# Optimization experiments

Hardware: AMD Instinct MI355X
Metric: run time of the kernel (lower is better)

## Reference

```python
import jax, jax.numpy as jnp
import numpy as np

B, D_IN, D_H, D_OUT = 1024, 1024, 4096, 1024
SPARSITY = 0.5  # fraction of weights KEPT (top-k)


def setup_inputs() -> dict:
    key = jax.random.key(0)
    ks = jax.random.split(key, 13)
    def kaiming(k, shape):
        fan_in = shape[-1] if len(shape) > 1 else shape[0]
        bound = 1.0 / np.sqrt(fan_in)
        return jax.random.uniform(k, shape, jnp.float32, -bound, bound)
    inp = {
        "x":   jax.random.normal(ks[0], (B, D_IN), jnp.float32),
        "W1":  kaiming(ks[1], (D_H, D_IN)),
        "b1":  kaiming(ks[2], (D_H,)),
        "W2":  kaiming(ks[3], (D_H, D_H)),
        "b2":  kaiming(ks[4], (D_H,)),
        "W3":  kaiming(ks[5], (D_OUT, D_H)),
        "b3":  kaiming(ks[6], (D_OUT,)),
        # scores: kaiming-uniform for weights, N(0, 0.01) for biases (as in Mask.__init__)
        "sW1": kaiming(ks[7], (D_H, D_IN)),
        "sb1": 0.01 * jax.random.normal(ks[8], (D_H,), jnp.float32),
        "sW2": kaiming(ks[9], (D_H, D_H)),
        "sb2": 0.01 * jax.random.normal(ks[10], (D_H,), jnp.float32),
        "sW3": kaiming(ks[11], (D_OUT, D_H)),
        "sb3": 0.01 * jax.random.normal(ks[12], (D_OUT,), jnp.float32),
    }
    return inp


def _global_masks(scores):
    """Single fused global top-k threshold mask (replaces O(P) redundant sorts).
    Bottom (1-SPARSITY) fraction (by value rank) -> 0, top SPARSITY fraction -> 1."""
    flat = jnp.concatenate([s.ravel() for s in scores])
    n = flat.shape[0]
    j = int((1.0 - SPARSITY) * n)  # number of zeroed entries
    idx = jnp.argsort(flat)
    bin_mask = jnp.zeros((n,), flat.dtype).at[idx[j:]].set(1.0)
    # straight-through: d(mask)/d(score) = 1 (GetSubnet_global.backward returns g)
    st_mask = bin_mask + flat - jax.lax.stop_gradient(flat)
    sizes = [int(np.prod(s.shape)) for s in scores]
    offs = np.concatenate([[0], np.cumsum(sizes)])
    return [st_mask[offs[i]:offs[i + 1]].reshape(scores[i].shape)
            for i in range(len(scores))]


def reference(x, W1, b1, W2, b2, W3, b3, sW1, sb1, sW2, sb2, sW3, sb3):
    masks = _global_masks([sW1, sb1, sW2, sb2, sW3, sb3])
    mW1, mb1, mW2, mb2, mW3, mb3 = masks
    # masked params, then MLP forward (torch Linear: y = x @ W.T + b)
    h = jax.nn.relu(x @ (W1 * mW1).T + b1 * mb1)
    h = jax.nn.relu(h @ (W2 * mW2).T + b2 * mb2)
    return h @ (W3 * mW3).T + b3 * mb3
```

## Files before the change

### kernel.cpp

```cpp
#include <hip/hip_runtime.h>
#include <hip/hip_bf16.h>
#include <stdint.h>


typedef __bf16 bf16_t;
typedef __bf16 bf16x4 __attribute__((ext_vector_type(4)));
typedef __bf16 bf16x8 __attribute__((ext_vector_type(8)));
typedef float  f32x4  __attribute__((ext_vector_type(4)));

using gvoid = const __attribute__((address_space(1))) void;
using svoid = __attribute__((address_space(3))) void;

#define O1 4194304L
#define O2 4198400L
#define O3 20975616L
#define O4 20979712L
#define O5 25174016L
#define N_TOT 25175040L
#define J_RANK 12587520u
#define CAND_CAP 4096

#define HIST_BLOCKS 512

#define WS_HIST 0u
#define WS_RES  32768u
#define WS_CNT  32784u
#define WS_CAND 32800u
#define WS_W1B  131072u
#define WS_B1F  8519680u
#define WS_W2B  8536064u
#define WS_B2F  42090496u
#define WS_W3B  42106880u
#define WS_B3F  50495488u
#define WS_H1F  50511872u
#define WS_H2F  58900480u
#define WS_FAST_END 67289088ull
#define WS_H1   131072u
#define WS_H2   8519680u

#define SWZ(row, chunk) ((((chunk) + ((row) >> 1)) & 3))

__device__ __forceinline__ unsigned int mono32(float f) {
    unsigned int u = __float_as_uint(f);
    return (u & 0x80000000u) ? ~u : (u | 0x80000000u);
}

__global__ __launch_bounds__(256) void zero_kernel(unsigned int* p, int n) {
    int i = blockIdx.x * 256 + threadIdx.x;
    if (i < n) p[i] = 0u;
}

__global__ __launch_bounds__(256) void cvt_x_kernel(const float* __restrict__ x,
                                                    bf16_t* __restrict__ xb, int n8) {
    int i = blockIdx.x * 256 + threadIdx.x;
    if (i < n8) {
        const float4 a = *(const float4*)(x + (size_t)i * 8);
        const float4 b = *(const float4*)(x + (size_t)i * 8 + 4);
        bf16x8 r;
        r[0] = (__bf16)a.x; r[1] = (__bf16)a.y; r[2] = (__bf16)a.z; r[3] = (__bf16)a.w;
        r[4] = (__bf16)b.x; r[5] = (__bf16)b.y; r[6] = (__bf16)b.z; r[7] = (__bf16)b.w;
        *(bf16x8*)(xb + (size_t)i * 8) = r;
    }
}

__device__ __forceinline__ void seg_lookup(long e,
    const float* s0, const float* s1, const float* s2,
    const float* s3, const float* s4, const float* s5,
    const float** sp, long* off) {
    if (e < O1)      { *sp = s0; *off = e; }
    else if (e < O2) { *sp = s1; *off = e - O1; }
    else if (e < O3) { *sp = s2; *off = e - O2; }
    else if (e < O4) { *sp = s3; *off = e - O3; }
    else if (e < O5) { *sp = s4; *off = e - O4; }
    else             { *sp = s5; *off = e - O5; }
}

__global__ __launch_bounds__(256) void hist_kernel(
    const float* s0, const float* s1, const float* s2,
    const float* s3, const float* s4, const float* s5,
    unsigned int* hb) {
    __shared__ unsigned int lh[8192];
    for (int i = threadIdx.x; i < 8192; i += 256) lh[i] = 0u;
    __syncthreads();
    const long ng = N_TOT / 4;
    for (long g = (long)blockIdx.x * 256 + threadIdx.x; g < ng;
         g += (long)gridDim.x * 256) {
        long e = g * 4;
        const float* sp; long o;
        seg_lookup(e, s0, s1, s2, s3, s4, s5, &sp, &o);
        float4 v = *(const float4*)(sp + o);
        atomicAdd(&lh[mono32(v.x) >> 19], 1u);
        atomicAdd(&lh[mono32(v.y) >> 19], 1u);
        atomicAdd(&lh[mono32(v.z) >> 19], 1u);
        atomicAdd(&lh[mono32(v.w) >> 19], 1u);
    }
    __syncthreads();
    unsigned int* dst = hb + (size_t)blockIdx.x * 8192;
    for (int i = threadIdx.x; i < 8192; i += 256) dst[i] = lh[i];
}

__global__ __launch_bounds__(256) void reduce_hist(const unsigned int* __restrict__ hb,
                                                   unsigned int* __restrict__ hist) {
    int b = blockIdx.x * 256 + threadIdx.x;
    unsigned int s = 0;
    for (int blk = 0; blk < HIST_BLOCKS; ++blk)
        s += hb[(size_t)blk * 8192 + b];
    hist[b] = s;
}

__global__ __launch_bounds__(256) void select_kernel(const unsigned int* hist,
                                                     unsigned int* res) {
    __shared__ unsigned int part[256];
    int tid = threadIdx.x;
    unsigned int s = 0;
    for (int b = tid * 32; b < tid * 32 + 32; ++b) s += hist[b];
    part[tid] = s;
    __syncthreads();
    if (tid == 0) {
        unsigned int acc = 0;
        for (int i = 0; i < 256; ++i) { unsigned int v = part[i]; part[i] = acc; acc += v; }
    }
    __syncthreads();
    unsigned int acc = part[tid];
    for (int b = tid * 32; b < tid * 32 + 32; ++b) {
        unsigned int h = hist[b];
        if (acc <= J_RANK && J_RANK < acc + h) {
            res[0] = (unsigned int)b;
            res[1] = acc;
            res[2] = J_RANK - acc;
        }
        acc += h;
    }
}

__global__ __launch_bounds__(256) void mask_apply_fast(
    const float* s0, const float* s1, const float* s2,
    const float* s3, const float* s4, const float* s5,
    const float* w0, const float* w1, const float* w2,
    const float* w3, const float* w4, const float* w5,
    bf16_t* W1b, float* b1f, bf16_t* W2b, float* b2f, bf16_t* W3b, float* b3f,
    const unsigned int* res, unsigned int* cand_cnt, unsigned long long* cand) {
    const unsigned int C = res[0];
    const long ng = N_TOT / 4;
    for (long g = (long)blockIdx.x * 256 + threadIdx.x; g < ng;
         g += (long)gridDim.x * 256) {
        long e = g * 4;
        const float* sp; long o;
        seg_lookup(e, s0, s1, s2, s3, s4, s5, &sp, &o);
        const float* wp;
        if (e < O1)      wp = w0;
        else if (e < O2) wp = w1;
        else if (e < O3) wp = w2;
        else if (e < O4) wp = w3;
        else if (e < O5) wp = w4;
        else             wp = w5;
        float4 sv = *(const float4*)(sp + o);
        float4 wv = *(const float4*)(wp + o);
#define PROC(comp, ci)                                                         \
        { unsigned int key = mono32(sv.comp); unsigned int kb = key >> 19;     \
          if (kb < C) wv.comp = 0.f;                                           \
          else if (kb == C) {                                                  \
              unsigned int slot = atomicAdd(cand_cnt, 1u);                     \
              if (slot < CAND_CAP)                                             \
                  cand[slot] = (((unsigned long long)key) << 32) |             \
                               (unsigned long long)(unsigned int)(e + ci);     \
          } }
        PROC(x, 0) PROC(y, 1) PROC(z, 2) PROC(w, 3)
#undef PROC
        if (e < O1) {
            bf16x4 b; b[0]=(__bf16)wv.x; b[1]=(__bf16)wv.y; b[2]=(__bf16)wv.z; b[3]=(__bf16)wv.w;
            *(bf16x4*)(W1b + o) = b;
        } else if (e < O2) {
            *(float4*)(b1f + o) = wv;
        } else if (e < O3) {
            bf16x4 b; b[0]=(__bf16)wv.x; b[1]=(__bf16)wv.y; b[2]=(__bf16)wv.z; b[3]=(__bf16)wv.w;
            *(bf16x4*)(W2b + o) = b;
        } else if (e < O4) {
            *(float4*)(b2f + o) = wv;
        } else if (e < O5) {
            bf16x4 b; b[0]=(__bf16)wv.x; b[1]=(__bf16)wv.y; b[2]=(__bf16)wv.z; b[3]=(__bf16)wv.w;
            *(bf16x4*)(W3b + o) = b;
        } else {
            *(float4*)(b3f + o) = wv;
        }
    }
}

__global__ __launch_bounds__(256) void finalize_fast(
    const unsigned int* res, const unsigned int* cand_cnt,
    const unsigned long long* cand,
    bf16_t* W1b, float* b1f, bf16_t* W2b, float* b2f, bf16_t* W3b, float* b3f) {
    __shared__ unsigned long long buf[CAND_CAP];
    int tid = threadIdx.x;
    unsigned int cnt = *cand_cnt; if (cnt > CAND_CAP) cnt = CAND_CAP;
    unsigned int need = res[2];   if (need > cnt) need = cnt;
    for (int i = tid; i < (int)cnt; i += 256) buf[i] = cand[i];
    __syncthreads();
    for (int i = tid; i < (int)cnt; i += 256) {
        unsigned long long me = buf[i];
        unsigned int rank = 0;
        for (unsigned int j = 0; j < cnt; ++j) rank += (buf[j] < me);
        if (rank < need) {
            long idx = (long)(unsigned int)(me & 0xFFFFFFFFu);
            if (idx < O1)      W1b[idx] = (__bf16)0.f;
            else if (idx < O2) b1f[idx - O1] = 0.f;
            else if (idx < O3) W2b[idx - O2] = (__bf16)0.f;
            else if (idx < O4) b2f[idx - O3] = 0.f;
            else if (idx < O5) W3b[idx - O4] = (__bf16)0.f;
            else               b3f[idx - O5] = 0.f;
        }
    }
}

__global__ __launch_bounds__(256) void mask_apply_kernel(
    const float* s0, const float* s1, const float* s2,
    const float* s3, const float* s4, const float* s5,
    float* w0, float* w1, float* w2, float* w3, float* w4, float* w5,
    const unsigned int* res, unsigned int* cand_cnt, unsigned long long* cand) {
    const unsigned int C = res[0];
    const long ng = N_TOT / 4;
    for (long g = (long)blockIdx.x * 256 + threadIdx.x; g < ng;
         g += (long)gridDim.x * 256) {
        long e = g * 4;
        const float* sp; long o;
        seg_lookup(e, s0, s1, s2, s3, s4, s5, &sp, &o);
        float* wp;
        if (e < O1)      wp = w0;
        else if (e < O2) wp = w1;
        else if (e < O3) wp = w2;
        else if (e < O4) wp = w3;
        else if (e < O5) wp = w4;
        else             wp = w5;
        float4 sv = *(const float4*)(sp + o);
        float4 wv = *(float4*)(wp + o);
#define PROC(comp, ci)                                                         \
        { unsigned int key = mono32(sv.comp); unsigned int kb = key >> 19;     \
          if (kb < C) wv.comp = 0.f;                                           \
          else if (kb == C) {                                                  \
              unsigned int slot = atomicAdd(cand_cnt, 1u);                     \
              if (slot < CAND_CAP)                                             \
                  cand[slot] = (((unsigned long long)key) << 32) |             \
                               (unsigned long long)(unsigned int)(e + ci);     \
          } }
        PROC(x, 0) PROC(y, 1) PROC(z, 2) PROC(w, 3)
#undef PROC
        *(float4*)(wp + o) = wv;
    }
}

__global__ __launch_bounds__(256) void finalize_kernel(
    const unsigned int* res, const unsigned int* cand_cnt,
    const unsigned long long* cand,
    float* w0, float* w1, float* w2, float* w3, float* w4, float* w5) {
    __shared__ unsigned long long buf[CAND_CAP];
    int tid = threadIdx.x;
    unsigned int cnt = *cand_cnt; if (cnt > CAND_CAP) cnt = CAND_CAP;
    unsigned int need = res[2];   if (need > cnt) need = cnt;
    for (int i = tid; i < (int)cnt; i += 256) buf[i] = cand[i];
    __syncthreads();
    for (int i = tid; i < (int)cnt; i += 256) {
        unsigned long long me = buf[i];
        unsigned int rank = 0;
        for (unsigned int j = 0; j < cnt; ++j) rank += (buf[j] < me);
        if (rank < need) {
            long idx = (long)(unsigned int)(me & 0xFFFFFFFFu);
            if (idx < O1)      w0[idx] = 0.f;
            else if (idx < O2) w1[idx - O1] = 0.f;
            else if (idx < O3) w2[idx - O2] = 0.f;
            else if (idx < O4) w3[idx - O3] = 0.f;
            else if (idx < O5) w4[idx - O4] = 0.f;
            else               w5[idx - O5] = 0.f;
        }
    }
}

__device__ __forceinline__ bf16x8 load8(const float* p) {
    float4 a = *(const float4*)p;
    float4 b = *(const float4*)(p + 4);
    bf16x8 r;
    r[0] = (__bf16)a.x; r[1] = (__bf16)a.y; r[2] = (__bf16)a.z; r[3] = (__bf16)a.w;
    r[4] = (__bf16)b.x; r[5] = (__bf16)b.y; r[6] = (__bf16)b.z; r[7] = (__bf16)b.w;
    return r;
}
__device__ __forceinline__ bf16x8 load8(const bf16_t* p) {
    return *(const bf16x8*)p;
}

template <int BM, int BN, bool RELU, typename TA, typename TB, typename TC>
__global__ __launch_bounds__(256) void gemm_bt(
    const TA* __restrict__ A, const TB* __restrict__ B,
    const float* __restrict__ bias, TC* __restrict__ C,
    int M, int N, int K) {
    constexpr int BK = 32;
    constexpr int WM = BM / 2, WN = BN / 2;
    constexpr int TM = WM / 16, TN = WN / 16;
    constexpr int CA = (BM * BK) / 8;
    constexpr int CB = (BN * BK) / 8;
    __shared__ __align__(16) bf16_t As[BM * BK];
    __shared__ __align__(16) bf16_t Bs[BN * BK];

    const int tid = threadIdx.x;
    const int w = tid >> 6, lane = tid & 63;
    const int quad = lane >> 4, l16 = lane & 15;
    const int wm = (w >> 1) * WM, wn = (w & 1) * WN;
    const int rowBase = blockIdx.y * BM;
    const int colBase = blockIdx.x * BN;

    f32x4 acc[TM][TN] = {};

    const TA* Ab = A + (size_t)rowBase * K;
    const TB* Bb = B + (size_t)colBase * K;

    for (int k0 = 0; k0 < K; k0 += BK) {
        __syncthreads();
#pragma unroll
        for (int c0 = 0; c0 < CA; c0 += 256) {
            int c = c0 + tid;
            int row = c >> 2, kc = c & 3;
            *(bf16x8*)&As[row * BK + SWZ(row, kc) * 8] =
                load8(Ab + (size_t)row * K + k0 + kc * 8);
        }
#pragma unroll
        for (int c0 = 0; c0 < CB; c0 += 256) {
            int c = c0 + tid;
            int row = c >> 2, kc = c & 3;
            *(bf16x8*)&Bs[row * BK + SWZ(row, kc) * 8] =
                load8(Bb + (size_t)row * K + k0 + kc * 8);
        }
        __syncthreads();
        bf16x8 af[TM], bfr[TN];
#pragma unroll
        for (int i = 0; i < TM; ++i) {
            int r = wm + i * 16 + l16;
            af[i] = *(const bf16x8*)&As[r * BK + SWZ(r, quad) * 8];
        }
#pragma unroll
        for (int j = 0; j < TN; ++j) {
            int r = wn + j * 16 + l16;
            bfr[j] = *(const bf16x8*)&Bs[r * BK + SWZ(r, quad) * 8];
        }
#pragma unroll
        for (int i = 0; i < TM; ++i)
#pragma unroll
            for (int j = 0; j < TN; ++j)
                acc[i][j] = __builtin_amdgcn_mfma_f32_16x16x32_bf16(
                    af[i], bfr[j], acc[i][j], 0, 0, 0);
    }

#pragma unroll
    for (int i = 0; i < TM; ++i) {
#pragma unroll
        for (int j = 0; j < TN; ++j) {
            int col = colBase + wn + j * 16 + l16;
            float bv = bias[col];
#pragma unroll
            for (int r = 0; r < 4; ++r) {
                int rowg = rowBase + wm + i * 16 + quad * 4 + r;
                float v = acc[i][j][r] + bv;
                if (RELU) v = v > 0.f ? v : 0.f;
                if constexpr (sizeof(TC) == 4)
                    C[(size_t)rowg * N + col] = v;
                else
                    C[(size_t)rowg * N + col] = (bf16_t)v;
            }
        }
    }
}

template <bool RELU, int SPLITK, typename TC>
__global__ __launch_bounds__(256) void gemm2ph(
    const bf16_t* __restrict__ A, const bf16_t* __restrict__ B,
    const float* __restrict__ bias, TC* __restrict__ C,
    int M, int N, int K, int gridX) {
    constexpr int BM = 64, BN = 128, BK = 32;
    constexpr int TM = 2, TN = 4;
    constexpr int CA = (BM * BK) / 8;
    constexpr int CB = (BN * BK) / 8;
    static_assert(CA == 256 && CB == 512, "staging assumes 3 loads/thread/step");
    __shared__ __align__(16) bf16_t As[2][BM * BK];
    __shared__ __align__(16) bf16_t Bs[2][BN * BK];

    const int tid = threadIdx.x;
    const int w = tid >> 6, lane = tid & 63;
    const int quad = lane >> 4, l16 = lane & 15;
    const int wm = (w >> 1) * 32, wn = (w & 1) * 64;

    const int nwg = gridX * (int)gridDim.y;
    const int wg = (int)blockIdx.y * gridX + (int)blockIdx.x;
    const int cpx = nwg >> 3;
    const int swz = (wg & 7) * cpx + (wg >> 3);
    const int bx = swz % gridX, by = swz / gridX;

    const int rowBase = by * BM;
    const int colBase = bx * BN;

    f32x4 acc[TM][TN] = {};

    const bf16_t* Ab = A + (size_t)rowBase * K;
    const bf16_t* Bb = B + (size_t)colBase * K;

    const int kPart = K / SPLITK;
    const int kBeg = (SPLITK > 1) ? (int)blockIdx.z * kPart : 0;
    const int nt = kPart / BK;

    const int rA = tid >> 2;
    const int lA = ((tid & 3) - (rA >> 1)) & 3;
    const int cB1 = tid + 256;
    const int rB1 = cB1 >> 2;
    const int lB1 = ((cB1 & 3) - (rB1 >> 1)) & 3;
    const bf16_t* aSrc  = Ab + (size_t)rA * K + lA * 8;
    const bf16_t* bSrc0 = Bb + (size_t)rA * K + lA * 8;
    const bf16_t* bSrc1 = Bb + (size_t)rB1 * K + lB1 * 8;

    auto stage = [&](int buf, int k0) {
        __builtin_amdgcn_global_load_lds((gvoid*)(aSrc + k0),
            (svoid*)(As[buf] + (size_t)tid * 8), 16, 0, 0);
        __builtin_amdgcn_global_load_lds((gvoid*)(bSrc0 + k0),
            (svoid*)(Bs[buf] + (size_t)tid * 8), 16, 0, 0);
        __builtin_amdgcn_global_load_lds((gvoid*)(bSrc1 + k0),
            (svoid*)(Bs[buf] + (size_t)cB1 * 8), 16, 0, 0);
    };
    auto compute = [&](int buf) {
        bf16x8 af[TM], bfr[TN];
#pragma unroll
        for (int i = 0; i < TM; ++i) {
            int r = wm + i * 16 + l16;
            af[i] = *(const bf16x8*)&As[buf][r * BK + SWZ(r, quad) * 8];
        }
#pragma unroll
        for (int j = 0; j < TN; ++j) {
            int r = wn + j * 16 + l16;
            bfr[j] = *(const bf16x8*)&Bs[buf][r * BK + SWZ(r, quad) * 8];
        }
#pragma unroll
        for (int i = 0; i < TM; ++i)
#pragma unroll
            for (int j = 0; j < TN; ++j)
                acc[i][j] = __builtin_amdgcn_mfma_f32_16x16x32_bf16(
                    af[i], bfr[j], acc[i][j], 0, 0, 0);
    };

    stage(0, kBeg);
    __syncthreads();
    for (int t = 0; t < nt - 1; ++t) {
        stage((t + 1) & 1, kBeg + (t + 1) * BK);
        compute(t & 1);
        __syncthreads();
    }
    compute((nt - 1) & 1);

#pragma unroll
    for (int i = 0; i < TM; ++i) {
#pragma unroll
        for (int j = 0; j < TN; ++j) {
            int col = colBase + wn + j * 16 + l16;
            float bv = (SPLITK == 1 || blockIdx.z == 0) ? bias[col] : 0.f;
#pragma unroll
            for (int r = 0; r < 4; ++r) {
                int rowg = rowBase + wm + i * 16 + quad * 4 + r;
                float v = acc[i][j][r] + bv;
                if constexpr (SPLITK == 1) {
                    if (RELU) v = v > 0.f ? v : 0.f;
                    if constexpr (sizeof(TC) == 4)
                        C[(size_t)rowg * N + col] = v;
                    else
                        C[(size_t)rowg * N + col] = (bf16_t)v;
                } else {
                    atomicAdd((float*)&C[(size_t)rowg * N + col], v);
                }
            }
        }
    }
}

extern "C" void kernel_launch(void* const* d_in, const int* in_sizes, int n_in,
                              void* d_out, int out_size, void* d_ws, size_t ws_size,
                              hipStream_t stream) {
    const float* x  = (const float*)d_in[0];
    float* W1 = (float*)d_in[1];
    float* b1 = (float*)d_in[2];
    float* W2 = (float*)d_in[3];
    float* b2 = (float*)d_in[4];
    float* W3 = (float*)d_in[5];
    float* b3 = (float*)d_in[6];
    const float* s0 = (const float*)d_in[7];
    const float* s1 = (const float*)d_in[8];
    const float* s2 = (const float*)d_in[9];
    const float* s3 = (const float*)d_in[10];
    const float* s4 = (const float*)d_in[11];
    const float* s5 = (const float*)d_in[12];

    uint8_t* ws = (uint8_t*)d_ws;
    unsigned int* hist = (unsigned int*)(ws + WS_HIST);
    unsigned int* res  = (unsigned int*)(ws + WS_RES);
    unsigned int* cnt  = (unsigned int*)(ws + WS_CNT);
    unsigned long long* cand = (unsigned long long*)(ws + WS_CAND);
    float* OUT = (float*)d_out;

    zero_kernel<<<33, 256, 0, stream>>>((unsigned int*)ws, 8200);

    if (ws_size >= WS_FAST_END) {
        bf16_t* W1b = (bf16_t*)(ws + WS_W1B);
        float*  b1f = (float*)(ws + WS_B1F);
        bf16_t* W2b = (bf16_t*)(ws + WS_W2B);
        float*  b2f = (float*)(ws + WS_B2F);
        bf16_t* W3b = (bf16_t*)(ws + WS_W3B);
        float*  b3f = (float*)(ws + WS_B3F);
        bf16_t* H1  = (bf16_t*)(ws + WS_H1F);
        bf16_t* H2  = (bf16_t*)(ws + WS_H2F);
        unsigned int* hb = (unsigned int*)(ws + WS_W2B);
        bf16_t* xb  = (bf16_t*)(ws + WS_H2F);

        hist_kernel<<<HIST_BLOCKS, 256, 0, stream>>>(s0, s1, s2, s3, s4, s5, hb);
        reduce_hist<<<32, 256, 0, stream>>>(hb, hist);
        select_kernel<<<1, 256, 0, stream>>>(hist, res);
        zero_kernel<<<4096, 256, 0, stream>>>((unsigned int*)OUT, 1048576);
        cvt_x_kernel<<<512, 256, 0, stream>>>(x, xb, 131072);
        mask_apply_fast<<<2048, 256, 0, stream>>>(
            s0, s1, s2, s3, s4, s5, W1, b1, W2, b2, W3, b3,
            W1b, b1f, W2b, b2f, W3b, b3f, res, cnt, cand);
        finalize_fast<<<1, 256, 0, stream>>>(res, cnt, cand,
                                             W1b, b1f, W2b, b2f, W3b, b3f);
        gemm2ph<true, 1, bf16_t>
            <<<dim3(32, 16), 256, 0, stream>>>(xb, W1b, b1f, H1, 1024, 4096, 1024, 32);
        gemm2ph<true, 1, bf16_t>
            <<<dim3(32, 16), 256, 0, stream>>>(H1, W2b, b2f, H2, 1024, 4096, 4096, 32);
        gemm2ph<false, 4, float>
            <<<dim3(8, 16, 4), 256, 0, stream>>>(H2, W3b, b3f, OUT, 1024, 1024, 4096, 8);
    } else {
        bf16_t* H1 = (bf16_t*)(ws + WS_H1);
        bf16_t* H2 = (bf16_t*)(ws + WS_H2);
        hist_kernel<<<1, 256, 0, stream>>>(s0, s1, s2, s3, s4, s5, hist);
        select_kernel<<<1, 256, 0, stream>>>(hist, res);
        mask_apply_kernel<<<2048, 256, 0, stream>>>(s0, s1, s2, s3, s4, s5,
                                                    W1, b1, W2, b2, W3, b3,
                                                    res, cnt, cand);
        finalize_kernel<<<1, 256, 0, stream>>>(res, cnt, cand,
                                               W1, b1, W2, b2, W3, b3);
        gemm_bt<64, 128, true, float, float, bf16_t>
            <<<dim3(32, 16), 256, 0, stream>>>(x, W1, b1, H1, 1024, 4096, 1024);
        gemm_bt<64, 128, true, bf16_t, float, bf16_t>
            <<<dim3(32, 16), 256, 0, stream>>>(H1, W2, b2, H2, 1024, 4096, 4096);
        gemm_bt<64, 64, false, bf16_t, float, float>
            <<<dim3(16, 16), 256, 0, stream>>>(H2, W3, b3, OUT, 1024, 1024, 4096);
    }
}
```

Before: 399.4 us.

## Fuse mask-prep kernels into one cooperative kernel and drop GEMM tile swizzle

The histogram, histogram reduction, threshold select, output zeroing, x-to-bf16 conversion, mask apply and candidate finalize steps now run as one cooperative kernel separated by grid-wide syncs. This removes several launches and inter-kernel gaps. The GEMM kernel drops its block-index swizzle and maps blocks directly to tiles, which may change L2 reuse. The fallback path switches to a multi-block histogram that accumulates with global atomics. In exchange the fused kernel relies on cooperative launch residency, with 1024 blocks using 32 KB of shared memory each. It also spends grid syncs where only one block or a few blocks do work.

```diff
diff --git a/kernel.cpp b/kernel.cpp
--- a/kernel.cpp
+++ b/kernel.cpp
@@ -1,6 +1,9 @@
 #include <hip/hip_runtime.h>
 #include <hip/hip_bf16.h>
+#include <hip/hip_cooperative_groups.h>
 #include <stdint.h>
+
+namespace cg = cooperative_groups;
 
 
 typedef __bf16 bf16_t;
@@ -20,7 +23,7 @@
 #define J_RANK 12587520u
 #define CAND_CAP 4096
 
-#define HIST_BLOCKS 512
+#define FUSED_BLOCKS 1024
 
 #define WS_HIST 0u
 #define WS_RES  32768u
@@ -50,19 +53,6 @@
     if (i < n) p[i] = 0u;
 }
 
-__global__ __launch_bounds__(256) void cvt_x_kernel(const float* __restrict__ x,
-                                                    bf16_t* __restrict__ xb, int n8) {
-    int i = blockIdx.x * 256 + threadIdx.x;
-    if (i < n8) {
-        const float4 a = *(const float4*)(x + (size_t)i * 8);
-        const float4 b = *(const float4*)(x + (size_t)i * 8 + 4);
-        bf16x8 r;
-        r[0] = (__bf16)a.x; r[1] = (__bf16)a.y; r[2] = (__bf16)a.z; r[3] = (__bf16)a.w;
-        r[4] = (__bf16)b.x; r[5] = (__bf16)b.y; r[6] = (__bf16)b.z; r[7] = (__bf16)b.w;
-        *(bf16x8*)(xb + (size_t)i * 8) = r;
-    }
-}
-
 __device__ __forceinline__ void seg_lookup(long e,
     const float* s0, const float* s1, const float* s2,
     const float* s3, const float* s4, const float* s5,
@@ -75,10 +65,166 @@
     else             { *sp = s5; *off = e - O5; }
 }
 
-__global__ __launch_bounds__(256) void hist_kernel(
+struct FusedArgs {
+    const float *s0, *s1, *s2, *s3, *s4, *s5;
+    const float *w0, *w1, *w2, *w3, *w4, *w5;
+    bf16_t* W1b; float* b1f; bf16_t* W2b; float* b2f; bf16_t* W3b; float* b3f;
+    unsigned int* hb;
+    unsigned int* hist;
+    unsigned int* res;
+    unsigned int* cnt;
+    unsigned long long* cand;
+    const float* x;
+    bf16_t* xb;
+    float* OUT;
+};
+
+__global__ __launch_bounds__(256, 4) void fused_mask(FusedArgs a) {
+    cg::grid_group grid = cg::this_grid();
+    __shared__ __align__(16) unsigned char shraw[32768];
+    const int tid = threadIdx.x;
+    const int bid = blockIdx.x;
+    const int nblk = gridDim.x;
+    const long gtid = (long)bid * 256 + tid;
+    const long nthr = (long)nblk * 256;
+    const long ng = N_TOT / 4;
+
+    unsigned int* lh = (unsigned int*)shraw;
+    for (int i = tid; i < 8192; i += 256) lh[i] = 0u;
+    if (gtid == 0) *a.cnt = 0u;
+    __syncthreads();
+    for (long g = gtid; g < ng; g += nthr) {
+        long e = g * 4;
+        const float* sp; long o;
+        seg_lookup(e, a.s0, a.s1, a.s2, a.s3, a.s4, a.s5, &sp, &o);
+        float4 v = *(const float4*)(sp + o);
+        atomicAdd(&lh[mono32(v.x) >> 19], 1u);
+        atomicAdd(&lh[mono32(v.y) >> 19], 1u);
+        atomicAdd(&lh[mono32(v.z) >> 19], 1u);
+        atomicAdd(&lh[mono32(v.w) >> 19], 1u);
+    }
+    __syncthreads();
+    {
+        unsigned int* dst = a.hb + (size_t)bid * 8192;
+        for (int i = tid; i < 8192; i += 256) dst[i] = lh[i];
+    }
+    grid.sync();
+
+    if (bid < 32) {
+        int b = bid * 256 + tid;
+        unsigned int s = 0;
+        for (int blk = 0; blk < nblk; ++blk)
+            s += a.hb[(size_t)blk * 8192 + b];
+        a.hist[b] = s;
+    }
+    grid.sync();
+
+    if (bid == 0) {
+        unsigned int* part = (unsigned int*)shraw;
+        unsigned int s = 0;
+        for (int b = tid * 32; b < tid * 32 + 32; ++b) s += a.hist[b];
+        part[tid] = s;
+        __syncthreads();
+        if (tid == 0) {
+            unsigned int acc = 0;
+            for (int i = 0; i < 256; ++i) { unsigned int v = part[i]; part[i] = acc; acc += v; }
+        }
+        __syncthreads();
+        unsigned int acc = part[tid];
+        for (int b = tid * 32; b < tid * 32 + 32; ++b) {
+            unsigned int h = a.hist[b];
+            if (acc <= J_RANK && J_RANK < acc + h) {
+                a.res[0] = (unsigned int)b;
+                a.res[1] = acc;
+                a.res[2] = J_RANK - acc;
+            }
+            acc += h;
+        }
+    }
+    grid.sync();
+
+    *(float4*)(a.OUT + gtid * 4) = make_float4(0.f, 0.f, 0.f, 0.f);
+    if (gtid < 131072) {
+        const float4 p = *(const float4*)(a.x + gtid * 8);
+        const float4 q = *(const float4*)(a.x + gtid * 8 + 4);
+        bf16x8 r;
+        r[0] = (__bf16)p.x; r[1] = (__bf16)p.y; r[2] = (__bf16)p.z; r[3] = (__bf16)p.w;
+        r[4] = (__bf16)q.x; r[5] = (__bf16)q.y; r[6] = (__bf16)q.z; r[7] = (__bf16)q.w;
+        *(bf16x8*)(a.xb + gtid * 8) = r;
+    }
+    {
+        const unsigned int C = a.res[0];
+        for (long g = gtid; g < ng; g += nthr) {
+            long e = g * 4;
+            const float* sp; long o;
+            seg_lookup(e, a.s0, a.s1, a.s2, a.s3, a.s4, a.s5, &sp, &o);
+            const float* wp;
+            if (e < O1)      wp = a.w0;
+            else if (e < O2) wp = a.w1;
+            else if (e < O3) wp = a.w2;
+            else if (e < O4) wp = a.w3;
+            else if (e < O5) wp = a.w4;
+            else             wp = a.w5;
+            float4 sv = *(const float4*)(sp + o);
+            float4 wv = *(const float4*)(wp + o);
+#define PROC(comp, ci)                                                         \
+            { unsigned int key = mono32(sv.comp); unsigned int kb = key >> 19; \
+              if (kb < C) wv.comp = 0.f;                                       \
+              else if (kb == C) {                                              \
+                  unsigned int slot = atomicAdd(a.cnt, 1u);                    \
+                  if (slot < CAND_CAP)                                         \
+                      a.cand[slot] = (((unsigned long long)key) << 32) |       \
+                                     (unsigned long long)(unsigned int)(e + ci);\
+              } }
+            PROC(x, 0) PROC(y, 1) PROC(z, 2) PROC(w, 3)
+#undef PROC
+            if (e < O1) {
+                bf16x4 b; b[0]=(__bf16)wv.x; b[1]=(__bf16)wv.y; b[2]=(__bf16)wv.z; b[3]=(__bf16)wv.w;
+                *(bf16x4*)(a.W1b + o) = b;
+            } else if (e < O2) {
+                *(float4*)(a.b1f + o) = wv;
+            } else if (e < O3) {
+                bf16x4 b; b[0]=(__bf16)wv.x; b[1]=(__bf16)wv.y; b[2]=(__bf16)wv.z; b[3]=(__bf16)wv.w;
+                *(bf16x4*)(a.W2b + o) = b;
+            } else if (e < O4) {
+                *(float4*)(a.b2f + o) = wv;
+            } else if (e < O5) {
+                bf16x4 b; b[0]=(__bf16)wv.x; b[1]=(__bf16)wv.y; b[2]=(__bf16)wv.z; b[3]=(__bf16)wv.w;
+                *(bf16x4*)(a.W3b + o) = b;
+            } else {
+                *(float4*)(a.b3f + o) = wv;
+            }
+        }
+    }
+    grid.sync();
+
+    if (bid == 0) {
+        unsigned long long* buf = (unsigned long long*)shraw;
+        unsigned int cnt = *a.cnt; if (cnt > CAND_CAP) cnt = CAND_CAP;
+        unsigned int need = a.res[2]; if (need > cnt) need = cnt;
+        for (int i = tid; i < (int)cnt; i += 256) buf[i] = a.cand[i];
+        __syncthreads();
+        for (int i = tid; i < (int)cnt; i += 256) {
+            unsigned long long me = buf[i];
+            unsigned int rank = 0;
+            for (unsigned int j = 0; j < cnt; ++j) rank += (buf[j] < me);
+            if (rank < need) {
+                long idx = (long)(unsigned int)(me & 0xFFFFFFFFu);
+                if (idx < O1)      a.W1b[idx] = (__bf16)0.f;
+                else if (idx < O2) a.b1f[idx - O1] = 0.f;
+                else if (idx < O3) a.W2b[idx - O2] = (__bf16)0.f;
+                else if (idx < O4) a.b2f[idx - O3] = 0.f;
+                else if (idx < O5) a.W3b[idx - O4] = (__bf16)0.f;
+                else               a.b3f[idx - O5] = 0.f;
+            }
+        }
+    }
+}
+
+__global__ __launch_bounds__(256) void hist_atomic_kernel(
     const float* s0, const float* s1, const float* s2,
     const float* s3, const float* s4, const float* s5,
-    unsigned int* hb) {
+    unsigned int* hist) {
     __shared__ unsigned int lh[8192];
     for (int i = threadIdx.x; i < 8192; i += 256) lh[i] = 0u;
     __syncthreads();
@@ -95,17 +241,10 @@
         atomicAdd(&lh[mono32(v.w) >> 19], 1u);
     }
     __syncthreads();
-    unsigned int* dst = hb + (size_t)blockIdx.x * 8192;
-    for (int i = threadIdx.x; i < 8192; i += 256) dst[i] = lh[i];
-}
-
-__global__ __launch_bounds__(256) void reduce_hist(const unsigned int* __restrict__ hb,
-                                                   unsigned int* __restrict__ hist) {
-    int b = blockIdx.x * 256 + threadIdx.x;
-    unsigned int s = 0;
-    for (int blk = 0; blk < HIST_BLOCKS; ++blk)
-        s += hb[(size_t)blk * 8192 + b];
-    hist[b] = s;
+    for (int i = threadIdx.x; i < 8192; i += 256) {
+        unsigned int c = lh[i];
+        if (c) atomicAdd(&hist[i], c);
+    }
 }
 
 __global__ __launch_bounds__(256) void select_kernel(const unsigned int* hist,
@@ -130,85 +269,6 @@
             res[2] = J_RANK - acc;
         }
         acc += h;
-    }
-}
-
-__global__ __launch_bounds__(256) void mask_apply_fast(
-    const float* s0, const float* s1, const float* s2,
-    const float* s3, const float* s4, const float* s5,
-    const float* w0, const float* w1, const float* w2,
-    const float* w3, const float* w4, const float* w5,
-    bf16_t* W1b, float* b1f, bf16_t* W2b, float* b2f, bf16_t* W3b, float* b3f,
-    const unsigned int* res, unsigned int* cand_cnt, unsigned long long* cand) {
-    const unsigned int C = res[0];
-    const long ng = N_TOT / 4;
-    for (long g = (long)blockIdx.x * 256 + threadIdx.x; g < ng;
-         g += (long)gridDim.x * 256) {
-        long e = g * 4;
-        const float* sp; long o;
-        seg_lookup(e, s0, s1, s2, s3, s4, s5, &sp, &o);
-        const float* wp;
-        if (e < O1)      wp = w0;
-        else if (e < O2) wp = w1;
-        else if (e < O3) wp = w2;
-        else if (e < O4) wp = w3;
-        else if (e < O5) wp = w4;
-        else             wp = w5;
-        float4 sv = *(const float4*)(sp + o);
-        float4 wv = *(const float4*)(wp + o);
-#define PROC(comp, ci)                                                         \
-        { unsigned int key = mono32(sv.comp); unsigned int kb = key >> 19;     \
-          if (kb < C) wv.comp = 0.f;                                           \
-          else if (kb == C) {                                                  \
-              unsigned int slot = atomicAdd(cand_cnt, 1u);                     \
-              if (slot < CAND_CAP)                                             \
-                  cand[slot] = (((unsigned long long)key) << 32) |             \
-                               (unsigned long long)(unsigned int)(e + ci);     \
-          } }
-        PROC(x, 0) PROC(y, 1) PROC(z, 2) PROC(w, 3)
-#undef PROC
-        if (e < O1) {
-            bf16x4 b; b[0]=(__bf16)wv.x; b[1]=(__bf16)wv.y; b[2]=(__bf16)wv.z; b[3]=(__bf16)wv.w;
-            *(bf16x4*)(W1b + o) = b;
-        } else if (e < O2) {
-            *(float4*)(b1f + o) = wv;
-        } else if (e < O3) {
-            bf16x4 b; b[0]=(__bf16)wv.x; b[1]=(__bf16)wv.y; b[2]=(__bf16)wv.z; b[3]=(__bf16)wv.w;
-            *(bf16x4*)(W2b + o) = b;
-        } else if (e < O4) {
-            *(float4*)(b2f + o) = wv;
-        } else if (e < O5) {
-            bf16x4 b; b[0]=(__bf16)wv.x; b[1]=(__bf16)wv.y; b[2]=(__bf16)wv.z; b[3]=(__bf16)wv.w;
-            *(bf16x4*)(W3b + o) = b;
-        } else {
-            *(float4*)(b3f + o) = wv;
-        }
-    }
-}
-
-__global__ __launch_bounds__(256) void finalize_fast(
-    const unsigned int* res, const unsigned int* cand_cnt,
-    const unsigned long long* cand,
-    bf16_t* W1b, float* b1f, bf16_t* W2b, float* b2f, bf16_t* W3b, float* b3f) {
-    __shared__ unsigned long long buf[CAND_CAP];
-    int tid = threadIdx.x;
-    unsigned int cnt = *cand_cnt; if (cnt > CAND_CAP) cnt = CAND_CAP;
-    unsigned int need = res[2];   if (need > cnt) need = cnt;
-    for (int i = tid; i < (int)cnt; i += 256) buf[i] = cand[i];
-    __syncthreads();
-    for (int i = tid; i < (int)cnt; i += 256) {
-        unsigned long long me = buf[i];
-        unsigned int rank = 0;
-        for (unsigned int j = 0; j < cnt; ++j) rank += (buf[j] < me);
-        if (rank < need) {
-            long idx = (long)(unsigned int)(me & 0xFFFFFFFFu);
-            if (idx < O1)      W1b[idx] = (__bf16)0.f;
-            else if (idx < O2) b1f[idx - O1] = 0.f;
-            else if (idx < O3) W2b[idx - O2] = (__bf16)0.f;
-            else if (idx < O4) b2f[idx - O3] = 0.f;
-            else if (idx < O5) W3b[idx - O4] = (__bf16)0.f;
-            else               b3f[idx - O5] = 0.f;
-        }
     }
 }
 
@@ -371,7 +431,7 @@
 __global__ __launch_bounds__(256) void gemm2ph(
     const bf16_t* __restrict__ A, const bf16_t* __restrict__ B,
     const float* __restrict__ bias, TC* __restrict__ C,
-    int M, int N, int K, int gridX) {
+    int M, int N, int K) {
     constexpr int BM = 64, BN = 128, BK = 32;
     constexpr int TM = 2, TN = 4;
     constexpr int CA = (BM * BK) / 8;
@@ -385,14 +445,8 @@
     const int quad = lane >> 4, l16 = lane & 15;
     const int wm = (w >> 1) * 32, wn = (w & 1) * 64;
 
-    const int nwg = gridX * (int)gridDim.y;
-    const int wg = (int)blockIdx.y * gridX + (int)blockIdx.x;
-    const int cpx = nwg >> 3;
-    const int swz = (wg & 7) * cpx + (wg >> 3);
-    const int bx = swz % gridX, by = swz / gridX;
-
-    const int rowBase = by * BM;
-    const int colBase = bx * BN;
+    const int rowBase = blockIdx.y * BM;
+    const int colBase = blockIdx.x * BN;
 
     f32x4 acc[TM][TN] = {};
 
@@ -497,8 +551,6 @@
     unsigned long long* cand = (unsigned long long*)(ws + WS_CAND);
     float* OUT = (float*)d_out;
 
-    zero_kernel<<<33, 256, 0, stream>>>((unsigned int*)ws, 8200);
-
     if (ws_size >= WS_FAST_END) {
         bf16_t* W1b = (bf16_t*)(ws + WS_W1B);
         float*  b1f = (float*)(ws + WS_B1F);
@@ -511,26 +563,29 @@
         unsigned int* hb = (unsigned int*)(ws + WS_W2B);
         bf16_t* xb  = (bf16_t*)(ws + WS_H2F);
 
-        hist_kernel<<<HIST_BLOCKS, 256, 0, stream>>>(s0, s1, s2, s3, s4, s5, hb);
-        reduce_hist<<<32, 256, 0, stream>>>(hb, hist);
-        select_kernel<<<1, 256, 0, stream>>>(hist, res);
-        zero_kernel<<<4096, 256, 0, stream>>>((unsigned int*)OUT, 1048576);
-        cvt_x_kernel<<<512, 256, 0, stream>>>(x, xb, 131072);
-        mask_apply_fast<<<2048, 256, 0, stream>>>(
-            s0, s1, s2, s3, s4, s5, W1, b1, W2, b2, W3, b3,
-            W1b, b1f, W2b, b2f, W3b, b3f, res, cnt, cand);
-        finalize_fast<<<1, 256, 0, stream>>>(res, cnt, cand,
-                                             W1b, b1f, W2b, b2f, W3b, b3f);
+        FusedArgs fa;
+        fa.s0 = s0; fa.s1 = s1; fa.s2 = s2; fa.s3 = s3; fa.s4 = s4; fa.s5 = s5;
+        fa.w0 = W1; fa.w1 = b1; fa.w2 = W2; fa.w3 = b2; fa.w4 = W3; fa.w5 = b3;
+        fa.W1b = W1b; fa.b1f = b1f; fa.W2b = W2b; fa.b2f = b2f;
+        fa.W3b = W3b; fa.b3f = b3f;
+        fa.hb = hb; fa.hist = hist; fa.res = res; fa.cnt = cnt; fa.cand = cand;
+        fa.x = x; fa.xb = xb; fa.OUT = OUT;
+        void* kargs[] = { (void*)&fa };
+        hipLaunchCooperativeKernel((const void*)fused_mask,
+                                   dim3(FUSED_BLOCKS), dim3(256),
+                                   kargs, 0, stream);
+
         gemm2ph<true, 1, bf16_t>
-            <<<dim3(32, 16), 256, 0, stream>>>(xb, W1b, b1f, H1, 1024, 4096, 1024, 32);
+            <<<dim3(32, 16), 256, 0, stream>>>(xb, W1b, b1f, H1, 1024, 4096, 1024);
         gemm2ph<true, 1, bf16_t>
-            <<<dim3(32, 16), 256, 0, stream>>>(H1, W2b, b2f, H2, 1024, 4096, 4096, 32);
+            <<<dim3(32, 16), 256, 0, stream>>>(H1, W2b, b2f, H2, 1024, 4096, 4096);
         gemm2ph<false, 4, float>
-            <<<dim3(8, 16, 4), 256, 0, stream>>>(H2, W3b, b3f, OUT, 1024, 1024, 4096, 8);
+            <<<dim3(8, 16, 4), 256, 0, stream>>>(H2, W3b, b3f, OUT, 1024, 1024, 4096);
     } else {
         bf16_t* H1 = (bf16_t*)(ws + WS_H1);
         bf16_t* H2 = (bf16_t*)(ws + WS_H2);
-        hist_kernel<<<1, 256, 0, stream>>>(s0, s1, s2, s3, s4, s5, hist);
+        zero_kernel<<<33, 256, 0, stream>>>((unsigned int*)ws, 8200);
+        hist_atomic_kernel<<<1024, 256, 0, stream>>>(s0, s1, s2, s3, s4, s5, hist);
         select_kernel<<<1, 256, 0, stream>>>(hist, res);
         mask_apply_kernel<<<2048, 256, 0, stream>>>(s0, s1, s2, s3, s4, s5,
                                                     W1, b1, W2, b2, W3, b3,
```

Result: slower. 956.1 us (+139.4%).
